# Optimization experiments

Measured on AMD Instinct MI355X. Metric: run time of the kernel, lower is better.

## Reference

```python
import jax, jax.numpy as jnp
import numpy as np

D = 1024  # input_size == context_size
B, SQ, SKV = 4, 2048, 2048


def setup_inputs() -> dict:
    key = jax.random.key(0)
    ks = jax.random.split(key, 8)
    s = 1.0 / np.sqrt(D)
    return {
        "x": jax.random.normal(ks[0], (B, SQ, D), jnp.float32),
        "context": jax.random.normal(ks[1], (B, SKV, D), jnp.float32),
        "Wq": jax.random.uniform(ks[2], (D, D), jnp.float32, -s, s),
        "bq": jnp.zeros((D,), jnp.float32),
        "Wk": jax.random.uniform(ks[3], (D, D), jnp.float32, -s, s),
        "bk": jnp.zeros((D,), jnp.float32),
        "Wv": jax.random.uniform(ks[4], (D, D), jnp.float32, -s, s),
        "bv": jnp.zeros((D,), jnp.float32),
    }


def reference(x, context, Wq, bq, Wk, bk, Wv, bv):
    # Linear layers (torch nn.Linear: y = x @ W^T + b; here W stored as [in, out])
    Q = x @ Wq + bq                  # [B, SQ, D]
    K = context @ Wk + bk            # [B, SKV, D]
    V = context @ Wv + bv            # [B, SKV, D]
    scale = 1.0 / np.sqrt(D).astype(np.float32)
    scores = jnp.einsum("bqd,bkd->bqk", Q, K) * scale  # [B, SQ, SKV]
    attn = jax.nn.softmax(scores, axis=-1)
    out = jnp.einsum("bqk,bkd->bqd", attn, V)          # [B, SQ, D]
    return out
```

## Files before the change

### kernel.cpp

```cpp
#include <hip/hip_runtime.h>
#include <cstdint>
#include <cstddef>

typedef __attribute__((ext_vector_type(8))) short short8;
typedef __attribute__((ext_vector_type(4))) float floatx4;
typedef __attribute__((ext_vector_type(16))) float floatx16;

__device__ __forceinline__ unsigned short f2bf(float f) {
    union { float f; unsigned int u; } v; v.f = f;
    unsigned int r = v.u + 0x7fffu + ((v.u >> 16) & 1u);
    return (unsigned short)(r >> 16);
}
__device__ __forceinline__ float bf2f(unsigned short h) {
    union { unsigned int u; float f; } v; v.u = ((unsigned int)h) << 16;
    return v.f;
}

__device__ __forceinline__ void glds16(const void* g, void* l) {
    __builtin_amdgcn_global_load_lds(
        (const __attribute__((address_space(1))) void*)g,
        (__attribute__((address_space(3))) void*)l, 16, 0, 0);
}

__device__ __forceinline__ void gemm_core(
    const unsigned short* __restrict__ Ab, int ldA,
    const unsigned short* __restrict__ Bb, int ldB,
    int K,
    unsigned short* __restrict__ As, unsigned short* __restrict__ Bs,
    floatx16 (&acc)[2][2])
{
    const int tid = threadIdx.x;
    const int wave = tid >> 6, lane = tid & 63;

    const unsigned short* gA[4];
    const unsigned short* gB[4];
#pragma unroll
    for (int i = 0; i < 4; ++i) {
        const int c = i * 256 + tid;
        const int row = c >> 3;
        const int l = (c & 7) ^ (row & 7);
        gA[i] = Ab + (size_t)row * ldA + l * 8;
        gB[i] = Bb + (size_t)row * ldB + l * 8;
    }
    const int arow = (wave >> 1) * 64 + (lane & 31);
    const int brow = (wave & 1) * 64 + (lane & 31);
    const int kg = lane >> 5;
    const int sw = lane & 7;
    const unsigned short* pa = As + arow * 64;
    const unsigned short* pb = Bs + brow * 64;

    for (int k0 = 0; k0 < K; k0 += 64) {
#pragma unroll
        for (int i = 0; i < 4; ++i)
            glds16(gA[i] + k0, As + (size_t)(i * 256 + wave * 64) * 8);
#pragma unroll
        for (int i = 0; i < 4; ++i)
            glds16(gB[i] + k0, Bs + (size_t)(i * 256 + wave * 64) * 8);
        __syncthreads();
#pragma unroll
        for (int s = 0; s < 4; ++s) {
            const int off = ((2 * s + kg) ^ sw) * 8;
            short8 a0 = *(const short8*)(pa + off);
            short8 a1 = *(const short8*)(pa + 32 * 64 + off);
            short8 b0 = *(const short8*)(pb + off);
            short8 b1 = *(const short8*)(pb + 32 * 64 + off);
            acc[0][0] = __builtin_amdgcn_mfma_f32_32x32x16_bf16(a0, b0, acc[0][0], 0, 0, 0);
            acc[0][1] = __builtin_amdgcn_mfma_f32_32x32x16_bf16(a0, b1, acc[0][1], 0, 0, 0);
            acc[1][0] = __builtin_amdgcn_mfma_f32_32x32x16_bf16(a1, b0, acc[1][0], 0, 0, 0);
            acc[1][1] = __builtin_amdgcn_mfma_f32_32x32x16_bf16(a1, b1, acc[1][1], 0, 0, 0);
        }
        __syncthreads();
    }
}

#define EPI_ROW(r, kg) (((r) & 3) + 8 * ((r) >> 2) + 4 * (kg))

__global__ __launch_bounds__(256) void prep_kernel(
    const float* __restrict__ x, const float* __restrict__ ctx,
    const float* __restrict__ Wq, const float* __restrict__ Wk, const float* __restrict__ Wv,
    unsigned short* __restrict__ xb, unsigned short* __restrict__ cb,
    unsigned short* __restrict__ Wt0, unsigned short* __restrict__ WtKV) {
    const int b = blockIdx.x;
    if (b < 16384) {
        int i = b * 256 + threadIdx.x;
        const float* in; unsigned short* out; int j;
        if (i < 2097152) { in = x; out = xb; j = i; }
        else { in = ctx; out = cb; j = i - 2097152; }
        float4 v = reinterpret_cast<const float4*>(in)[j];
        ushort4 o;
        o.x = f2bf(v.x); o.y = f2bf(v.y); o.z = f2bf(v.z); o.w = f2bf(v.w);
        reinterpret_cast<ushort4*>(out)[j] = o;
    } else {
        __shared__ float tile[32][33];
        const int z = b - 16384;
        const int w = z >> 10, t = z & 1023;
        const float* in = (w == 0) ? Wq : (w == 1) ? Wk : Wv;
        unsigned short* out = (w == 0) ? Wt0 : (w == 1) ? WtKV : (WtKV + 1024 * 1024);
        const int c0 = (t & 31) * 32, r0 = (t >> 5) * 32;
        const int tx = threadIdx.x & 31, ty = threadIdx.x >> 5;
#pragma unroll
        for (int j = 0; j < 4; ++j)
            tile[ty + j * 8][tx] = in[(size_t)(r0 + ty + j * 8) * 1024 + c0 + tx];
        __syncthreads();
#pragma unroll
        for (int j = 0; j < 4; ++j)
            out[(size_t)(c0 + ty + j * 8) * 1024 + r0 + tx] = f2bf(tile[tx][ty + j * 8]);
    }
}

__global__ __launch_bounds__(256, 3) void qkv_kernel(
    const unsigned short* __restrict__ xb, const unsigned short* __restrict__ cb,
    const unsigned short* __restrict__ WtQ, const unsigned short* __restrict__ WtKV,
    const float* __restrict__ bq, const float* __restrict__ bk, const float* __restrict__ bv,
    unsigned short* __restrict__ Qb, unsigned short* __restrict__ Kb,
    unsigned short* __restrict__ Vt) {
    __shared__ unsigned short As[128 * 64];
    __shared__ unsigned short Bs[128 * 64];
    const int vb = blockIdx.x;
    const bool isQ = vb < 512;
    int by, bxcol;
    const unsigned short *A, *B;
    if (isQ) {
        by = vb >> 3; const int bx = vb & 7; bxcol = bx * 128;
        A = xb + (size_t)by * 128 * 1024;
        B = WtQ + (size_t)bx * 128 * 1024;
    } else {
        const int v = vb - 512;
        by = v >> 4; const int bx = v & 15; bxcol = bx * 128;
        A = cb + (size_t)by * 128 * 1024;
        B = WtKV + (size_t)bx * 128 * 1024;
    }
    floatx16 acc[2][2];
#pragma unroll
    for (int i = 0; i < 2; ++i)
#pragma unroll
        for (int j = 0; j < 2; ++j)
#pragma unroll
            for (int r = 0; r < 16; ++r) acc[i][j][r] = 0.f;

    gemm_core(A, 1024, B, 1024, 1024, As, Bs, acc);

    const int wave = threadIdx.x >> 6, lane = threadIdx.x & 63;
    const int kg = lane >> 5;
    const int cm = by * 128 + (wave >> 1) * 64;
    const int cn = bxcol + (wave & 1) * 64 + (lane & 31);
    if (isQ || bxcol < 1024) {
        unsigned short* O = isQ ? Qb : Kb;
        const float* bias = isQ ? bq : bk;
#pragma unroll
        for (int nt = 0; nt < 2; ++nt) {
            const int col = cn + nt * 32;
            const float bvv = bias[col];
#pragma unroll
            for (int mt = 0; mt < 2; ++mt)
#pragma unroll
                for (int r = 0; r < 16; ++r) {
                    const int row = cm + mt * 32 + EPI_ROW(r, kg);
                    O[(size_t)row * 1024 + col] = f2bf(acc[mt][nt][r] + bvv);
                }
        }
    } else {
#pragma unroll
        for (int nt = 0; nt < 2; ++nt) {
            const int colv = cn + nt * 32 - 1024;
            const float bvv = bv[colv];
#pragma unroll
            for (int mt = 0; mt < 2; ++mt) {
                const int rowg = cm + mt * 32 + 4 * kg;
                const int b = rowg >> 11, qb = rowg & 2047;
#pragma unroll
                for (int g = 0; g < 4; ++g) {
                    const int q = qb + 8 * g;
                    ushort4 u;
                    u.x = f2bf(acc[mt][nt][g * 4 + 0] + bvv);
                    u.y = f2bf(acc[mt][nt][g * 4 + 1] + bvv);
                    u.z = f2bf(acc[mt][nt][g * 4 + 2] + bvv);
                    u.w = f2bf(acc[mt][nt][g * 4 + 3] + bvv);
                    *reinterpret_cast<ushort4*>(Vt + (size_t)b * 2097152 + (size_t)colv * 2048 + q) = u;
                }
            }
        }
    }
}

__global__ __launch_bounds__(256, 3) void qkt_kernel(
    const unsigned short* __restrict__ Qb, const unsigned short* __restrict__ Kb,
    unsigned short* __restrict__ Sb) {
    __shared__ unsigned short As[128 * 64];
    __shared__ unsigned short Bs[128 * 64];
    const int z = blockIdx.z;
    const unsigned short* A = Qb + (size_t)z * 2048 * 1024 + (size_t)blockIdx.y * 128 * 1024;
    const unsigned short* B = Kb + (size_t)z * 2048 * 1024 + (size_t)blockIdx.x * 128 * 1024;
    floatx16 acc[2][2];
#pragma unroll
    for (int i = 0; i < 2; ++i)
#pragma unroll
        for (int j = 0; j < 2; ++j)
#pragma unroll
            for (int r = 0; r < 16; ++r) acc[i][j][r] = 0.f;

    gemm_core(A, 1024, B, 1024, 1024, As, Bs, acc);

    const int wave = threadIdx.x >> 6, lane = threadIdx.x & 63;
    const int kg = lane >> 5;
    unsigned short* C = Sb + (size_t)z * 2048 * 2048;
    const int cm = blockIdx.y * 128 + (wave >> 1) * 64;
    const int cn = blockIdx.x * 128 + (wave & 1) * 64 + (lane & 31);
#pragma unroll
    for (int nt = 0; nt < 2; ++nt)
#pragma unroll
        for (int mt = 0; mt < 2; ++mt)
#pragma unroll
            for (int r = 0; r < 16; ++r) {
                const int row = cm + mt * 32 + EPI_ROW(r, kg);
                C[(size_t)row * 2048 + cn + nt * 32] = f2bf(acc[mt][nt][r] * 0.03125f);
            }
}

__global__ __launch_bounds__(256, 3) void pv_kernel(
    const unsigned short* __restrict__ Sb, const unsigned short* __restrict__ Vt,
    float* __restrict__ out) {
    __shared__ unsigned short As[128 * 64];
    __shared__ unsigned short Bs[128 * 64];
    const int z = blockIdx.z;
    const unsigned short* A = Sb + (size_t)z * 2048 * 2048 + (size_t)blockIdx.y * 128 * 2048;
    const unsigned short* B = Vt + (size_t)z * 1024 * 2048 + (size_t)blockIdx.x * 128 * 2048;
    floatx16 acc[2][2];
#pragma unroll
    for (int i = 0; i < 2; ++i)
#pragma unroll
        for (int j = 0; j < 2; ++j)
#pragma unroll
            for (int r = 0; r < 16; ++r) acc[i][j][r] = 0.f;

    gemm_core(A, 2048, B, 2048, 2048, As, Bs, acc);

    const int wave = threadIdx.x >> 6, lane = threadIdx.x & 63;
    const int kg = lane >> 5;
    float* C = out + (size_t)z * 2048 * 1024;
    const int cm = blockIdx.y * 128 + (wave >> 1) * 64;
    const int cn = blockIdx.x * 128 + (wave & 1) * 64 + (lane & 31);
#pragma unroll
    for (int nt = 0; nt < 2; ++nt)
#pragma unroll
        for (int mt = 0; mt < 2; ++mt)
#pragma unroll
            for (int r = 0; r < 16; ++r) {
                const int row = cm + mt * 32 + EPI_ROW(r, kg);
                C[(size_t)row * 1024 + cn + nt * 32] = acc[mt][nt][r];
            }
}

__global__ __launch_bounds__(256) void softmax_kernel(unsigned short* __restrict__ S) {
    unsigned short* row = S + (size_t)blockIdx.x * 2048;
    const int t = threadIdx.x;
    ushort4 u0 = reinterpret_cast<const ushort4*>(row)[t * 2];
    ushort4 u1 = reinterpret_cast<const ushort4*>(row)[t * 2 + 1];
    float v[8];
    v[0] = bf2f(u0.x); v[1] = bf2f(u0.y); v[2] = bf2f(u0.z); v[3] = bf2f(u0.w);
    v[4] = bf2f(u1.x); v[5] = bf2f(u1.y); v[6] = bf2f(u1.z); v[7] = bf2f(u1.w);

    float lm = v[0];
#pragma unroll
    for (int j = 1; j < 8; ++j) lm = fmaxf(lm, v[j]);
#pragma unroll
    for (int o = 32; o > 0; o >>= 1) lm = fmaxf(lm, __shfl_xor(lm, o));

    __shared__ float red[8];
    const int wv = t >> 6;
    if ((t & 63) == 0) red[wv] = lm;
    __syncthreads();
    const float rm = fmaxf(fmaxf(red[0], red[1]), fmaxf(red[2], red[3]));

    float s = 0.f;
#pragma unroll
    for (int j = 0; j < 8; ++j) { v[j] = __expf(v[j] - rm); s += v[j]; }
#pragma unroll
    for (int o = 32; o > 0; o >>= 1) s += __shfl_xor(s, o);
    if ((t & 63) == 0) red[4 + wv] = s;
    __syncthreads();
    const float inv = 1.f / (red[4] + red[5] + red[6] + red[7]);

    ushort4 o0, o1;
    o0.x = f2bf(v[0] * inv); o0.y = f2bf(v[1] * inv);
    o0.z = f2bf(v[2] * inv); o0.w = f2bf(v[3] * inv);
    o1.x = f2bf(v[4] * inv); o1.y = f2bf(v[5] * inv);
    o1.z = f2bf(v[6] * inv); o1.w = f2bf(v[7] * inv);
    reinterpret_cast<ushort4*>(row)[t * 2] = o0;
    reinterpret_cast<ushort4*>(row)[t * 2 + 1] = o1;
}

extern "C" void kernel_launch(void* const* d_in, const int* in_sizes, int n_in,
                              void* d_out, int out_size, void* d_ws, size_t ws_size,
                              hipStream_t stream) {
    const float* x   = (const float*)d_in[0];
    const float* ctx = (const float*)d_in[1];
    const float* Wq  = (const float*)d_in[2];
    const float* bq  = (const float*)d_in[3];
    const float* Wk  = (const float*)d_in[4];
    const float* bk  = (const float*)d_in[5];
    const float* Wv  = (const float*)d_in[6];
    const float* bv  = (const float*)d_in[7];
    float* out = (float*)d_out;

    const size_t MB = 1024 * 1024;
    char* ws = (char*)d_ws;
    unsigned short* xb   = (unsigned short*)(ws + 0 * MB);
    unsigned short* cb   = (unsigned short*)(ws + 16 * MB);
    unsigned short* Qb   = (unsigned short*)(ws + 32 * MB);
    unsigned short* Kb   = (unsigned short*)(ws + 48 * MB);
    unsigned short* Vt   = (unsigned short*)(ws + 64 * MB);
    unsigned short* Wt0  = (unsigned short*)(ws + 80 * MB);
    unsigned short* WtKV = (unsigned short*)(ws + 82 * MB);
    unsigned short* Sb   = (unsigned short*)(ws + 86 * MB);

    prep_kernel<<<16384 + 3072, 256, 0, stream>>>(x, ctx, Wq, Wk, Wv, xb, cb, Wt0, WtKV);
    qkv_kernel<<<1536, 256, 0, stream>>>(xb, cb, Wt0, WtKV, bq, bk, bv, Qb, Kb, Vt);
    qkt_kernel<<<dim3(16, 16, 4), 256, 0, stream>>>(Qb, Kb, Sb);
    softmax_kernel<<<8192, 256, 0, stream>>>(Sb);
    pv_kernel<<<dim3(8, 16, 4), 256, 0, stream>>>(Sb, Vt, out);
}
```

Baseline: 301.6 us.

## Load QK^T fragments directly from global memory and refine LDS swizzle

The QK^T kernel drops LDS staging and syncthreads and instead has each wave load MFMA operand fragments straight from global memory into registers, double-buffered across iterations. The shared gemm_core also gets a new XOR swizzle that mixes higher row bits, plus a different offset for the second 32-row half, to cut LDS bank conflicts in the other GEMMs. The direct global loads give up LDS data sharing between waves, so each Q/K fragment is fetched twice from cache, and the short8 loads per lane are strided and may coalesce poorly.

```diff
diff --git a/kernel.cpp b/kernel.cpp
--- a/kernel.cpp
+++ b/kernel.cpp
@@ -3,7 +3,6 @@
 #include <cstddef>
 
 typedef __attribute__((ext_vector_type(8))) short short8;
-typedef __attribute__((ext_vector_type(4))) float floatx4;
 typedef __attribute__((ext_vector_type(16))) float floatx16;
 
 __device__ __forceinline__ unsigned short f2bf(float f) {
@@ -21,6 +20,8 @@
         (const __attribute__((address_space(1))) void*)g,
         (__attribute__((address_space(3))) void*)l, 16, 0, 0);
 }
+
+#define EPI_ROW(r, kg) (((r) & 3) + 8 * ((r) >> 2) + 4 * (kg))
 
 __device__ __forceinline__ void gemm_core(
     const unsigned short* __restrict__ Ab, int ldA,
@@ -38,14 +39,14 @@
     for (int i = 0; i < 4; ++i) {
         const int c = i * 256 + tid;
         const int row = c >> 3;
-        const int l = (c & 7) ^ (row & 7);
+        const int l = (c & 7) ^ ((row ^ (row >> 3)) & 7);
         gA[i] = Ab + (size_t)row * ldA + l * 8;
         gB[i] = Bb + (size_t)row * ldB + l * 8;
     }
     const int arow = (wave >> 1) * 64 + (lane & 31);
     const int brow = (wave & 1) * 64 + (lane & 31);
     const int kg = lane >> 5;
-    const int sw = lane & 7;
+    const int sw = (lane & 7) ^ ((lane >> 3) & 3);
     const unsigned short* pa = As + arow * 64;
     const unsigned short* pb = Bs + brow * 64;
 
@@ -59,11 +60,12 @@
         __syncthreads();
 #pragma unroll
         for (int s = 0; s < 4; ++s) {
-            const int off = ((2 * s + kg) ^ sw) * 8;
-            short8 a0 = *(const short8*)(pa + off);
-            short8 a1 = *(const short8*)(pa + 32 * 64 + off);
-            short8 b0 = *(const short8*)(pb + off);
-            short8 b1 = *(const short8*)(pb + 32 * 64 + off);
+            const int o0 = ((2 * s + kg) ^ sw) * 8;
+            const int o1 = o0 ^ 32;
+            short8 a0 = *(const short8*)(pa + o0);
+            short8 a1 = *(const short8*)(pa + 32 * 64 + o1);
+            short8 b0 = *(const short8*)(pb + o0);
+            short8 b1 = *(const short8*)(pb + 32 * 64 + o1);
             acc[0][0] = __builtin_amdgcn_mfma_f32_32x32x16_bf16(a0, b0, acc[0][0], 0, 0, 0);
             acc[0][1] = __builtin_amdgcn_mfma_f32_32x32x16_bf16(a0, b1, acc[0][1], 0, 0, 0);
             acc[1][0] = __builtin_amdgcn_mfma_f32_32x32x16_bf16(a1, b0, acc[1][0], 0, 0, 0);
@@ -72,8 +74,6 @@
         __syncthreads();
     }
 }
-
-#define EPI_ROW(r, kg) (((r) & 3) + 8 * ((r) >> 2) + 4 * (kg))
 
 __global__ __launch_bounds__(256) void prep_kernel(
     const float* __restrict__ x, const float* __restrict__ ctx,
@@ -183,14 +183,19 @@
     }
 }
 
-__global__ __launch_bounds__(256, 3) void qkt_kernel(
+__global__ __launch_bounds__(256) void qkt_kernel(
     const unsigned short* __restrict__ Qb, const unsigned short* __restrict__ Kb,
     unsigned short* __restrict__ Sb) {
-    __shared__ unsigned short As[128 * 64];
-    __shared__ unsigned short Bs[128 * 64];
     const int z = blockIdx.z;
-    const unsigned short* A = Qb + (size_t)z * 2048 * 1024 + (size_t)blockIdx.y * 128 * 1024;
-    const unsigned short* B = Kb + (size_t)z * 2048 * 1024 + (size_t)blockIdx.x * 128 * 1024;
+    const int wave = threadIdx.x >> 6, lane = threadIdx.x & 63;
+    const int kg = lane >> 5, ml = lane & 31;
+    const unsigned short* pa0 = Qb + (size_t)z * 2097152 +
+        (size_t)(blockIdx.y * 128 + (wave >> 1) * 64 + ml) * 1024 + kg * 8;
+    const unsigned short* pa1 = pa0 + 32 * 1024;
+    const unsigned short* pb0 = Kb + (size_t)z * 2097152 +
+        (size_t)(blockIdx.x * 128 + (wave & 1) * 64 + ml) * 1024 + kg * 8;
+    const unsigned short* pb1 = pb0 + 32 * 1024;
+
     floatx16 acc[2][2];
 #pragma unroll
     for (int i = 0; i < 2; ++i)
@@ -199,11 +204,54 @@
 #pragma unroll
             for (int r = 0; r < 16; ++r) acc[i][j][r] = 0.f;
 
-    gemm_core(A, 1024, B, 1024, 1024, As, Bs, acc);
-
-    const int wave = threadIdx.x >> 6, lane = threadIdx.x & 63;
-    const int kg = lane >> 5;
-    unsigned short* C = Sb + (size_t)z * 2048 * 2048;
+    short8 fa[2][2][2], fb[2][2][2];
+#pragma unroll
+    for (int s = 0; s < 2; ++s) {
+        fa[0][0][s] = *(const short8*)(pa0 + s * 16);
+        fa[0][1][s] = *(const short8*)(pa1 + s * 16);
+        fb[0][0][s] = *(const short8*)(pb0 + s * 16);
+        fb[0][1][s] = *(const short8*)(pb1 + s * 16);
+    }
+    const int NIT = 32;
+    for (int it = 0; it < NIT; it += 2) {
+        {
+            const int off = (it + 1) * 32;
+#pragma unroll
+            for (int s = 0; s < 2; ++s) {
+                fa[1][0][s] = *(const short8*)(pa0 + off + s * 16);
+                fa[1][1][s] = *(const short8*)(pa1 + off + s * 16);
+                fb[1][0][s] = *(const short8*)(pb0 + off + s * 16);
+                fb[1][1][s] = *(const short8*)(pb1 + off + s * 16);
+            }
+        }
+#pragma unroll
+        for (int s = 0; s < 2; ++s) {
+            acc[0][0] = __builtin_amdgcn_mfma_f32_32x32x16_bf16(fa[0][0][s], fb[0][0][s], acc[0][0], 0, 0, 0);
+            acc[0][1] = __builtin_amdgcn_mfma_f32_32x32x16_bf16(fa[0][0][s], fb[0][1][s], acc[0][1], 0, 0, 0);
+            acc[1][0] = __builtin_amdgcn_mfma_f32_32x32x16_bf16(fa[0][1][s], fb[0][0][s], acc[1][0], 0, 0, 0);
+            acc[1][1] = __builtin_amdgcn_mfma_f32_32x32x16_bf16(fa[0][1][s], fb[0][1][s], acc[1][1], 0, 0, 0);
+        }
+        if (it + 2 < NIT) {
+            const int off = (it + 2) * 32;
+#pragma unroll
+            for (int s = 0; s < 2; ++s) {
+                fa[0][0][s] = *(const short8*)(pa0 + off + s * 16);
+                fa[0][1][s] = *(const short8*)(pa1 + off + s * 16);
+                fb[0][0][s] = *(const short8*)(pb0 + off + s * 16);
+                fb[0][1][s] = *(const short8*)(pb1 + off + s * 16);
+            }
+        }
+#pragma unroll
+        for (int s = 0; s < 2; ++s) {
+            acc[0][0] = __builtin_amdgcn_mfma_f32_32x32x16_bf16(fa[1][0][s], fb[1][0][s], acc[0][0], 0, 0, 0);
+            acc[0][1] = __builtin_amdgcn_mfma_f32_32x32x16_bf16(fa[1][0][s], fb[1][1][s], acc[0][1], 0, 0, 0);
+            acc[1][0] = __builtin_amdgcn_mfma_f32_32x32x16_bf16(fa[1][1][s], fb[1][0][s], acc[1][0], 0, 0, 0);
+            acc[1][1] = __builtin_amdgcn_mfma_f32_32x32x16_bf16(fa[1][1][s], fb[1][1][s], acc[1][1], 0, 0, 0);
+        }
+    }
+
+    const int kg2 = lane >> 5;
+    unsigned short* C = Sb + (size_t)z * 4194304;
     const int cm = blockIdx.y * 128 + (wave >> 1) * 64;
     const int cn = blockIdx.x * 128 + (wave & 1) * 64 + (lane & 31);
 #pragma unroll
@@ -212,7 +260,7 @@
         for (int mt = 0; mt < 2; ++mt)
 #pragma unroll
             for (int r = 0; r < 16; ++r) {
-                const int row = cm + mt * 32 + EPI_ROW(r, kg);
+                const int row = cm + mt * 32 + EPI_ROW(r, kg2);
                 C[(size_t)row * 2048 + cn + nt * 32] = f2bf(acc[mt][nt][r] * 0.03125f);
             }
 }
@@ -223,8 +271,8 @@
     __shared__ unsigned short As[128 * 64];
     __shared__ unsigned short Bs[128 * 64];
     const int z = blockIdx.z;
-    const unsigned short* A = Sb + (size_t)z * 2048 * 2048 + (size_t)blockIdx.y * 128 * 2048;
-    const unsigned short* B = Vt + (size_t)z * 1024 * 2048 + (size_t)blockIdx.x * 128 * 2048;
+    const unsigned short* A = Sb + (size_t)z * 4194304 + (size_t)blockIdx.y * 128 * 2048;
+    const unsigned short* B = Vt + (size_t)z * 2097152 + (size_t)blockIdx.x * 128 * 2048;
     floatx16 acc[2][2];
 #pragma unroll
     for (int i = 0; i < 2; ++i)
@@ -237,7 +285,7 @@
 
     const int wave = threadIdx.x >> 6, lane = threadIdx.x & 63;
     const int kg = lane >> 5;
-    float* C = out + (size_t)z * 2048 * 1024;
+    float* C = out + (size_t)z * 2097152;
     const int cm = blockIdx.y * 128 + (wave >> 1) * 64;
     const int cn = blockIdx.x * 128 + (wave & 1) * 64 + (lane & 31);
 #pragma unroll
```

After: 380.2 us. +26.1%, slower.
